# Optimization experiments

Measured on AMD Instinct MI355X. Metric: run time of the kernel, lower is better.

The kernel has to match this reference:

```python
import jax, jax.numpy as jnp
import numpy as np

K = 256       # num states
M = 2         # markov order
D = 256       # lemb_size
V = 50000     # ntypes (vocab)
T = 512
B = 256
Kp1 = K + 1
EPS = 1e-5
INIT = 0.1


def _layernorm(h, g, b):
    mu = h.mean(-1, keepdims=True)
    var = ((h - mu) ** 2).mean(-1, keepdims=True)
    return (h - mu) / jnp.sqrt(var + EPS) * g + b


def setup_inputs() -> dict:
    key = jax.random.key(0)
    ks = jax.random.split(key, 12)
    u = lambda k, shp: jax.random.uniform(k, shp, jnp.float32, -INIT, INIT)
    return {
        "x": jax.random.randint(ks[0], (T, B), 0, V, dtype=jnp.int32),
        "z": jax.random.randint(ks[1], (T, B), 0, K, dtype=jnp.int32),
        "lembs": u(ks[2], (K, D)),
        "tlembs": u(ks[3], (Kp1, D)),
        "dec_W": u(ks[4], (V, D)),
        "dec_b": jnp.zeros((V,), jnp.float32),
        "em_W": u(ks[5], (D, D)),
        "em_bias": jnp.zeros((D,), jnp.float32),
        "em_g": jnp.ones((D,), jnp.float32),
        "em_beta": jnp.zeros((D,), jnp.float32),
        "td_W": u(ks[6], (K, M * D)),
        "td_b": jnp.zeros((K,), jnp.float32),
        "tm_W": u(ks[7], (M * D, M * D)),
        "tm_bias": jnp.zeros((M * D,), jnp.float32),
        "tn_g": jnp.ones((M * D,), jnp.float32),
        "tn_beta": jnp.zeros((M * D,), jnp.float32),
    }


def reference(x, z, lembs, tlembs, dec_W, dec_b, em_W, em_bias, em_g, em_beta,
              td_W, td_b, tm_W, tm_bias, tn_g, tn_beta):
    # --- emission distribution: K x V log-normalized ---
    h = _layernorm(lembs + jax.nn.relu(lembs @ em_W.T + em_bias), em_g, em_beta)
    emdist = jax.nn.log_softmax(h @ dec_W.T + dec_b, axis=1)  # (K, V)

    # --- transition distribution: (Kp1^M, K) log-normalized ---
    # cartesian product of label embeddings, row-major: row r <-> (i_0,...,i_{M-1})
    idx = jnp.indices((Kp1,) * M).reshape(M, -1)                 # (M, Kp1^M)
    cat = tlembs[idx].transpose(1, 0, 2).reshape(-1, M * D)      # (Kp1^M, M*D)
    th = _layernorm(cat + jax.nn.relu(cat @ tm_W.T + tm_bias), tn_g, tn_beta)
    transdist = jax.nn.log_softmax(th @ td_W.T + td_b, axis=1)   # (Kp1^M, K)

    # --- log_joint ---
    xlps = emdist.T[x]                                           # (T, B, K)
    emlps = jnp.take_along_axis(xlps, z[..., None].astype(jnp.int32), axis=2)[..., 0].sum(0)  # (B,)

    zpad = jnp.concatenate([jnp.full((M, B), K, dtype=z.dtype), z], axis=0)  # (T+M, B)
    win = jnp.stack([zpad[m:m + T] for m in range(M + 1)], 0)    # (M+1, T, B)
    lin = win[0]
    for m in range(1, M):
        lin = lin * Kp1 + win[m]                                 # row index into (Kp1^M, K)
    trans_lps = transdist[lin, win[M]]                           # (T, B)
    return emlps + trans_lps.sum(0)                              # (B,)
```

## Files before the change

kernel.cpp:

```cpp
#include <hip/hip_runtime.h>

#define Kst 256
#define Dd 256
#define Vv 50000
#define VPAD 50176
#define Tt 512
#define Bb 256
#define KP1 257
#define MD 512
#define NROWS (KP1*KP1)
#define EPSf 1e-5f

#define VB2 196
#define NP1 (VB2*4)
#define NTR ((NROWS+31)/32)
#define EMB 800

typedef __attribute__((ext_vector_type(8))) short short8;
typedef __attribute__((ext_vector_type(4))) float f32x4;
typedef __attribute__((ext_vector_type(4))) unsigned u32x4;
typedef __attribute__((ext_vector_type(2))) unsigned u32x2;

__device__ __forceinline__ unsigned short f2bf(float f) {
    unsigned u = __builtin_bit_cast(unsigned, f);
    unsigned r = (u + 0x7fffu + ((u >> 16) & 1u)) >> 16;
    return (unsigned short)r;
}
__device__ __forceinline__ float bf2f(unsigned short u) {
    return __builtin_bit_cast(float, ((unsigned)u) << 16);
}
__device__ __forceinline__ unsigned bfpack(float lo, float hi) {
    return __builtin_amdgcn_perm(__builtin_bit_cast(unsigned, hi),
                                 __builtin_bit_cast(unsigned, lo), 0x07060302u);
}
__device__ __forceinline__ unsigned f2bf2(float lo, float hi) {
    return (unsigned)f2bf(lo) | ((unsigned)f2bf(hi) << 16);
}

__global__ __launch_bounds__(256) void k_pack(
    const float* __restrict__ dec_W, unsigned short* __restrict__ dwP,
    const float* __restrict__ em_W, unsigned short* __restrict__ emWP,
    const float* __restrict__ tm_W, unsigned short* __restrict__ tmWP,
    const float* __restrict__ td_W, const float* __restrict__ tn_g,
    const float* __restrict__ tn_beta, const float* __restrict__ td_b,
    unsigned short* __restrict__ tdwg_bf, float* __restrict__ Gt,
    float* __restrict__ Bt)
{
    __shared__ short pl[64][266];
    int bid = blockIdx.x;
    int tid = threadIdx.x, lane = tid & 63, wv = tid >> 6;

    if (bid < 784) {
        int vb2 = bid >> 2, c = bid & 3;
        int base_row = vb2*256 + c*64;
        #pragma unroll 4
        for (int i = 0; i < 16; ++i) {
            int row = wv*16 + i;
            int grow = base_row + row; if (grow > Vv-1) grow = Vv-1;
            float4 f = ((const float4*)(dec_W + (size_t)grow*Dd))[lane];
            u32x2 w; w.x = bfpack(f.x, f.y); w.y = bfpack(f.z, f.w);
            *(u32x2*)&pl[row][lane*4] = w;
        }
        __syncthreads();
        #pragma unroll
        for (int i = 0; i < 8; ++i) {
            short8 val = *(const short8*)&pl[(lane & 15)*4 + wv][i*32 + (lane >> 4)*8];
            *(short8*)(dwP + ((size_t)vb2*8192 + (size_t)i*1024
                              + (c*4 + wv)*64 + lane)*8) = val;
        }
        return;
    }
    if (bid < 788) {
        int jc = bid - 784;
        #pragma unroll 4
        for (int i = 0; i < 16; ++i) {
            int row = wv*16 + i;
            int j = jc*64 + row;
            float4 f = ((const float4*)(em_W + (size_t)j*Dd))[lane];
            u32x2 w; w.x = bfpack(f.x, f.y); w.y = bfpack(f.z, f.w);
            *(u32x2*)&pl[row][lane*4] = w;
        }
        __syncthreads();
        #pragma unroll
        for (int i = 0; i < 8; ++i) {
            short8 val = *(const short8*)&pl[(lane & 15)*4 + wv][i*32 + (lane >> 4)*8];
            *(short8*)(emWP + ((size_t)(i*16 + jc*4 + wv)*64 + lane)*8) = val;
        }
        return;
    }
    if (bid < 804) {
        int idx = bid - 788;
        int jb = idx >> 3, t = idx & 7, jc = t >> 1, kh = t & 1;
        #pragma unroll 4
        for (int i = 0; i < 16; ++i) {
            int row = wv*16 + i;
            int j = jb*256 + jc*64 + row;
            float4 f = ((const float4*)(tm_W + (size_t)j*MD + kh*256))[lane];
            u32x2 w; w.x = bfpack(f.x, f.y); w.y = bfpack(f.z, f.w);
            *(u32x2*)&pl[row][lane*4] = w;
        }
        __syncthreads();
        #pragma unroll
        for (int i = 0; i < 8; ++i) {
            int ksG = kh*8 + i;
            short8 val = *(const short8*)&pl[(lane & 15)*4 + wv][i*32 + (lane >> 4)*8];
            *(short8*)(tmWP + ((size_t)((jb*16 + ksG)*16 + jc*4 + wv)*64 + lane)*8) = val;
        }
        return;
    }
    {
        int c = (bid - 804)*4 + wv;
        const float4* w4 = (const float4*)(td_W + (size_t)c*MD);
        const float4* g4 = (const float4*)tn_g;
        const float4* b4 = (const float4*)tn_beta;
        float sg = 0.f, sb = 0.f;
        short8 o;
        #pragma unroll
        for (int u = 0; u < 2; ++u) {
            int j4 = lane*2 + u;
            float4 w = w4[j4], g = g4[j4], bt = b4[j4];
            sg += w.x*g.x + w.y*g.y + w.z*g.z + w.w*g.w;
            sb += w.x*bt.x + w.y*bt.y + w.z*bt.z + w.w*bt.w;
            o[u*4+0] = (short)f2bf(w.x*g.x);
            o[u*4+1] = (short)f2bf(w.y*g.y);
            o[u*4+2] = (short)f2bf(w.z*g.z);
            o[u*4+3] = (short)f2bf(w.w*g.w);
        }
        {
            int wvv = c >> 6, l15v = (c >> 2) & 15, ctv = c & 3;
            int ksv = lane >> 2, qv = lane & 3;
            *(short8*)(tdwg_bf +
                ((((size_t)wvv*16 + ksv)*4 + ctv)*64 + (qv*16 + l15v))*8) = o;
        }
        #pragma unroll
        for (int dd = 32; dd > 0; dd >>= 1) {
            sg += __shfl_xor(sg, dd);
            sb += __shfl_xor(sb, dd);
        }
        if (lane == 0) { Gt[c] = sg; Bt[c] = sb + td_b[c]; }
    }
}

__global__ __launch_bounds__(256) void k_hP2(
    const float* __restrict__ lembs, const float* __restrict__ em_bias,
    const float* __restrict__ em_g, const float* __restrict__ em_beta,
    unsigned short* __restrict__ h_bf, const float* __restrict__ tlembs,
    float* __restrict__ P0, float* __restrict__ P1,
    const unsigned short* __restrict__ emWP, const unsigned short* __restrict__ tmWP)
{
    __shared__ short ta[32][264];
    __shared__ float lsep[4][32][2];
    __shared__ float musig[32][2];
    int bid = blockIdx.x;
    int tid = threadIdx.x, lane = tid & 63, wv = tid >> 6;
    int l15 = lane & 15, q = lane >> 4;

    int job, r0, cb;
    const float* Arow;
    const short8* bb8;
    if (bid < 8) {
        job = 0; r0 = bid*32; cb = 0;
        Arow = lembs;
        bb8 = (const short8*)emWP + (size_t)(wv*4)*64 + lane;
    } else {
        int b2 = bid - 8;
        int half = b2 / 18;
        int b3 = b2 % 18;
        job = 1 + half;
        r0 = (b3 >> 1) * 32;
        cb = (b3 & 1) * 256;
        int jb = cb >> 8;
        Arow = tlembs;
        bb8 = (const short8*)tmWP + ((size_t)(jb*16 + half*8)*16 + wv*4)*64 + lane;
    }

    {
        int row = tid >> 3, seg = (tid & 7) * 32;
        int r = r0 + row;
        if (r > 256) r = 256;
        const float4* s4 = (const float4*)(Arow + (size_t)r*Dd + seg);
        #pragma unroll
        for (int u = 0; u < 4; ++u) {
            float4 f0 = s4[u*2], f1 = s4[u*2+1];
            u32x4 pk;
            pk.x = bfpack(f0.x, f0.y);
            pk.y = bfpack(f0.z, f0.w);
            pk.z = bfpack(f1.x, f1.y);
            pk.w = bfpack(f1.z, f1.w);
            *(short8*)&ta[row][seg + u*8] = __builtin_bit_cast(short8, pk);
        }
    }
    __syncthreads();

    f32x4 acc[2][4];
    #pragma unroll
    for (int rt = 0; rt < 2; ++rt)
        #pragma unroll
        for (int ct = 0; ct < 4; ++ct)
            acc[rt][ct] = (f32x4){0.f,0.f,0.f,0.f};
    #pragma unroll
    for (int ks = 0; ks < 8; ++ks) {
        short8 a0 = *(const short8*)&ta[ 0 + l15][ks*32 + q*8];
        short8 a1 = *(const short8*)&ta[16 + l15][ks*32 + q*8];
        short8 b0 = bb8[(ks*16 + 0)*64];
        short8 b1 = bb8[(ks*16 + 1)*64];
        short8 b2 = bb8[(ks*16 + 2)*64];
        short8 b3 = bb8[(ks*16 + 3)*64];
        acc[0][0] = __builtin_amdgcn_mfma_f32_16x16x32_bf16(a0, b0, acc[0][0], 0,0,0);
        acc[1][0] = __builtin_amdgcn_mfma_f32_16x16x32_bf16(a1, b0, acc[1][0], 0,0,0);
        acc[0][1] = __builtin_amdgcn_mfma_f32_16x16x32_bf16(a0, b1, acc[0][1], 0,0,0);
        acc[1][1] = __builtin_amdgcn_mfma_f32_16x16x32_bf16(a1, b1, acc[1][1], 0,0,0);
        acc[0][2] = __builtin_amdgcn_mfma_f32_16x16x32_bf16(a0, b2, acc[0][2], 0,0,0);
        acc[1][2] = __builtin_amdgcn_mfma_f32_16x16x32_bf16(a1, b2, acc[1][2], 0,0,0);
        acc[0][3] = __builtin_amdgcn_mfma_f32_16x16x32_bf16(a0, b3, acc[0][3], 0,0,0);
        acc[1][3] = __builtin_amdgcn_mfma_f32_16x16x32_bf16(a1, b3, acc[1][3], 0,0,0);
    }

    if (job != 0) {
        float* Pd = (job == 1) ? P0 : P1;
        #pragma unroll
        for (int rt = 0; rt < 2; ++rt) {
            #pragma unroll
            for (int reg = 0; reg < 4; ++reg) {
                int r = r0 + rt*16 + q*4 + reg;
                if (r < KP1) {
                    float4 o;
                    o.x = acc[rt][0][reg]; o.y = acc[rt][1][reg];
                    o.z = acc[rt][2][reg]; o.w = acc[rt][3][reg];
                    *(float4*)(Pd + (size_t)r*MD + cb + wv*64 + l15*4) = o;
                }
            }
        }
        return;
    }

    float4 bias4 = *(const float4*)(em_bias + wv*64 + l15*4);
    #pragma unroll
    for (int rt = 0; rt < 2; ++rt) {
        #pragma unroll
        for (int reg = 0; reg < 4; ++reg) {
            int r = r0 + rt*16 + q*4 + reg;
            float4 lv = *(const float4*)(lembs + (size_t)r*Dd + wv*64 + l15*4);
            acc[rt][0][reg] = lv.x + fmaxf(acc[rt][0][reg] + bias4.x, 0.f);
            acc[rt][1][reg] = lv.y + fmaxf(acc[rt][1][reg] + bias4.y, 0.f);
            acc[rt][2][reg] = lv.z + fmaxf(acc[rt][2][reg] + bias4.z, 0.f);
            acc[rt][3][reg] = lv.w + fmaxf(acc[rt][3][reg] + bias4.w, 0.f);
        }
    }
    #pragma unroll
    for (int rt = 0; rt < 2; ++rt) {
        #pragma unroll
        for (int reg = 0; reg < 4; ++reg) {
            float s  = ((acc[rt][0][reg] + acc[rt][1][reg]) + (acc[rt][2][reg] + acc[rt][3][reg]));
            float ss = ((acc[rt][0][reg]*acc[rt][0][reg] + acc[rt][1][reg]*acc[rt][1][reg])
                      + (acc[rt][2][reg]*acc[rt][2][reg] + acc[rt][3][reg]*acc[rt][3][reg]));
            s  += __shfl_xor(s, 1);  ss += __shfl_xor(ss, 1);
            s  += __shfl_xor(s, 2);  ss += __shfl_xor(ss, 2);
            s  += __shfl_xor(s, 4);  ss += __shfl_xor(ss, 4);
            s  += __shfl_xor(s, 8);  ss += __shfl_xor(ss, 8);
            if (l15 == 0) {
                int rw = rt*16 + q*4 + reg;
                lsep[wv][rw][0] = s;
                lsep[wv][rw][1] = ss;
            }
        }
    }
    __syncthreads();
    if (tid < 32) {
        float s  = (lsep[0][tid][0] + lsep[1][tid][0]) + (lsep[2][tid][0] + lsep[3][tid][0]);
        float ss = (lsep[0][tid][1] + lsep[1][tid][1]) + (lsep[2][tid][1] + lsep[3][tid][1]);
        float mu = s * (1.f/Dd);
        musig[tid][0] = mu;
        musig[tid][1] = rsqrtf(ss*(1.f/Dd) - mu*mu + EPSf);
    }
    __syncthreads();
    float4 g4  = *(const float4*)(em_g + wv*64 + l15*4);
    float4 be4 = *(const float4*)(em_beta + wv*64 + l15*4);
    #pragma unroll
    for (int rt = 0; rt < 2; ++rt) {
        #pragma unroll
        for (int reg = 0; reg < 4; ++reg) {
            int rw = rt*16 + q*4 + reg;
            int r = r0 + rw;
            float mu = musig[rw][0], rs = musig[rw][1];
            float e0 = (acc[rt][0][reg] - mu)*rs*g4.x + be4.x;
            float e1 = (acc[rt][1][reg] - mu)*rs*g4.y + be4.y;
            float e2 = (acc[rt][2][reg] - mu)*rs*g4.z + be4.z;
            float e3 = (acc[rt][3][reg] - mu)*rs*g4.w + be4.w;
            u32x2 p;
            p.x = f2bf2(e0, e1);
            p.y = f2bf2(e2, e3);
            *(u32x2*)(h_bf + (size_t)r*Dd + wv*64 + l15*4) = p;
        }
    }
}

union SMemU {
    struct { short hs[64][264]; } em;
    struct { short th[32][520]; float musig[32][2]; float lsep[4][32][2]; } tr;
};

__global__ __launch_bounds__(256, 4) void k_emtrans(
    const unsigned short* __restrict__ dwP, const float* __restrict__ dec_b,
    const unsigned short* __restrict__ h_bf, float* __restrict__ part1,
    unsigned short* __restrict__ E2,
    const float* __restrict__ tlembs, const float* __restrict__ P0,
    const float* __restrict__ P1, const float* __restrict__ tm_bias,
    const short* __restrict__ tdwg_bf, const float* __restrict__ Gt,
    const float* __restrict__ Bt, float* __restrict__ lse_t,
    unsigned short* __restrict__ Td)
{
    __shared__ SMemU sm;
    int bid = blockIdx.x;
    int tid = threadIdx.x, lane = tid & 63, wv = tid >> 6;
    int l15 = lane & 15, q = lane >> 4;

    if (bid < EMB) {
        int xcd = bid & 7, slot = bid >> 3;
        int g2 = slot >> 2, kg = slot & 3;
        int vb = g2*8 + xcd;
        if (vb >= VB2) return;
        short (*hs)[264] = sm.em.hs;

        {
            int row = tid >> 2, c0 = (tid & 3) * 64;
            const short8* src = (const short8*)(h_bf + (size_t)(kg*64 + row)*Dd + c0);
            #pragma unroll
            for (int u = 0; u < 8; ++u)
                *(short8*)&hs[row][c0 + u*8] = src[u];
        }
        __syncthreads();

        f32x4 acc[4][4];
        #pragma unroll
        for (int mt = 0; mt < 4; ++mt)
            #pragma unroll
            for (int ct = 0; ct < 4; ++ct)
                acc[mt][ct] = (f32x4){0.f,0.f,0.f,0.f};

        const short8* bb8 = (const short8*)dwP + ((size_t)vb*8*16 + wv*4)*64 + lane;
        short8 Bf[3][4];
        #define LDB_EM(slot_, kk) { \
            Bf[slot_][0] = bb8[((kk)*16 + 0)*64]; \
            Bf[slot_][1] = bb8[((kk)*16 + 1)*64]; \
            Bf[slot_][2] = bb8[((kk)*16 + 2)*64]; \
            Bf[slot_][3] = bb8[((kk)*16 + 3)*64]; }
        LDB_EM(0, 0)
        LDB_EM(1, 1)
        #pragma unroll
        for (int ks = 0; ks < 8; ++ks) {
            if (ks < 6) LDB_EM((ks+2)%3, ks+2)
            short8 a[4];
            #pragma unroll
            for (int mt = 0; mt < 4; ++mt)
                a[mt] = *(const short8*)&hs[mt*16 + l15][ks*32 + q*8];
            #pragma unroll
            for (int mt = 0; mt < 4; ++mt)
                #pragma unroll
                for (int ct = 0; ct < 4; ++ct)
                    acc[mt][ct] = __builtin_amdgcn_mfma_f32_16x16x32_bf16(a[mt], Bf[ks%3][ct], acc[mt][ct], 0,0,0);
        }
        #undef LDB_EM

        int vcol[4]; bool vok[4];
        #pragma unroll
        for (int ct = 0; ct < 4; ++ct) {
            int v = vb*256 + wv*64 + l15*4 + ct;
            vok[ct] = (v < Vv);
            vcol[ct] = v < Vv ? v : Vv-1;
        }
        #pragma unroll
        for (int ct = 0; ct < 4; ++ct) {
            if (vok[ct]) {
                float db = dec_b[vcol[ct]];
                #pragma unroll
                for (int mt = 0; mt < 4; ++mt)
                    #pragma unroll
                    for (int reg = 0; reg < 4; ++reg)
                        acc[mt][ct][reg] += db;
            } else {
                #pragma unroll
                for (int mt = 0; mt < 4; ++mt)
                    #pragma unroll
                    for (int reg = 0; reg < 4; ++reg)
                        acc[mt][ct][reg] = -1e30f;
            }
        }
        #pragma unroll
        for (int mt = 0; mt < 4; ++mt) {
            #pragma unroll
            for (int reg = 0; reg < 4; ++reg) {
                int k = kg*64 + mt*16 + q*4 + reg;
                u32x2 p;
                p.x = f2bf2(acc[mt][0][reg], acc[mt][1][reg]);
                p.y = f2bf2(acc[mt][2][reg], acc[mt][3][reg]);
                *(u32x2*)(E2 + (size_t)k*VPAD + vb*256 + wv*64 + l15*4) = p;
            }
        }
        #pragma unroll
        for (int mt = 0; mt < 4; ++mt) {
            #pragma unroll
            for (int reg = 0; reg < 4; ++reg) {
                float s = (__expf(acc[mt][0][reg]) + __expf(acc[mt][1][reg]))
                        + (__expf(acc[mt][2][reg]) + __expf(acc[mt][3][reg]));
                s += __shfl_xor(s, 1);
                s += __shfl_xor(s, 2);
                s += __shfl_xor(s, 4);
                s += __shfl_xor(s, 8);
                if (l15 == 0) {
                    int k = kg*64 + mt*16 + q*4 + reg;
                    part1[(size_t)(vb*4 + wv)*256 + k] = s;
                }
            }
        }
        return;
    }

    int tr_id = bid - EMB;
    if (tr_id >= NTR) return;
    short (*th)[520]   = sm.tr.th;
    float (*musig)[2]  = sm.tr.musig;
    float (*lsep)[32][2] = sm.tr.lsep;
    int r0 = tr_id * 32;

    {
        const float4* bias0 = (const float4*)tm_bias;
        const float4* bias1 = (const float4*)(tm_bias + 256);
        float4 c0 = bias0[lane], c1 = bias1[lane];
        int i0a[8], i1a[8];
        #pragma unroll
        for (int i = 0; i < 8; ++i) {
            int r = r0 + wv*8 + i; if (r >= NROWS) r = NROWS - 1;
            i0a[i] = r / KP1; i1a[i] = r - i0a[i]*KP1;
        }
        #define ROWBODY(i, A0, B0, T0, A1, B1, T1) { \
            int row = wv*8 + (i); \
            float v0 = (T0).x + fmaxf((A0).x+(B0).x+c0.x, 0.f); \
            float v1 = (T0).y + fmaxf((A0).y+(B0).y+c0.y, 0.f); \
            float v2 = (T0).z + fmaxf((A0).z+(B0).z+c0.z, 0.f); \
            float v3 = (T0).w + fmaxf((A0).w+(B0).w+c0.w, 0.f); \
            float v4 = (T1).x + fmaxf((A1).x+(B1).x+c1.x, 0.f); \
            float v5 = (T1).y + fmaxf((A1).y+(B1).y+c1.y, 0.f); \
            float v6 = (T1).z + fmaxf((A1).z+(B1).z+c1.z, 0.f); \
            float v7 = (T1).w + fmaxf((A1).w+(B1).w+c1.w, 0.f); \
            u32x2 p0; p0.x = bfpack(v0, v1); p0.y = bfpack(v2, v3); \
            u32x2 p1; p1.x = bfpack(v4, v5); p1.y = bfpack(v6, v7); \
            *(u32x2*)&th[row][lane*4]       = p0; \
            *(u32x2*)&th[row][256 + lane*4] = p1; \
            float s  = ((v0+v1)+(v2+v3)) + ((v4+v5)+(v6+v7)); \
            float ss = ((v0*v0+v1*v1)+(v2*v2+v3*v3)) + ((v4*v4+v5*v5)+(v6*v6+v7*v7)); \
            _Pragma("unroll") \
            for (int d = 1; d < 64; d <<= 1) { \
                s  += __shfl_xor(s, d); \
                ss += __shfl_xor(ss, d); \
            } \
            if (lane == 0) { \
                float mu = s * (1.f/MD); \
                musig[row][0] = mu; \
                musig[row][1] = rsqrtf(ss*(1.f/MD) - mu*mu + EPSf); \
            } }

        if (i0a[0] == i0a[7]) {
            float4 A0 = ((const float4*)(P0 + (size_t)i0a[0]*MD))[lane];
            float4 A1 = ((const float4*)(P0 + (size_t)i0a[0]*MD + 256))[lane];
            float4 T0 = ((const float4*)(tlembs + (size_t)i0a[0]*Dd))[lane];
            #pragma unroll
            for (int i = 0; i < 8; ++i) {
                float4 b0 = ((const float4*)(P1 + (size_t)i1a[i]*MD))[lane];
                float4 b1 = ((const float4*)(P1 + (size_t)i1a[i]*MD + 256))[lane];
                float4 t1 = ((const float4*)(tlembs + (size_t)i1a[i]*Dd))[lane];
                ROWBODY(i, A0, b0, T0, A1, b1, t1)
            }
        } else {
            #pragma unroll
            for (int i = 0; i < 8; ++i) {
                float4 A0 = ((const float4*)(P0 + (size_t)i0a[i]*MD))[lane];
                float4 A1 = ((const float4*)(P0 + (size_t)i0a[i]*MD + 256))[lane];
                float4 T0 = ((const float4*)(tlembs + (size_t)i0a[i]*Dd))[lane];
                float4 b0 = ((const float4*)(P1 + (size_t)i1a[i]*MD))[lane];
                float4 b1 = ((const float4*)(P1 + (size_t)i1a[i]*MD + 256))[lane];
                float4 t1 = ((const float4*)(tlembs + (size_t)i1a[i]*Dd))[lane];
                ROWBODY(i, A0, b0, T0, A1, b1, t1)
            }
        }
        #undef ROWBODY
    }
    __syncthreads();

    f32x4 acc[2][4];
    #pragma unroll
    for (int rt = 0; rt < 2; ++rt)
        #pragma unroll
        for (int ct = 0; ct < 4; ++ct)
            acc[rt][ct] = (f32x4){0.f, 0.f, 0.f, 0.f};
    const short* bb = tdwg_bf + (size_t)wv*32768 + (size_t)lane*8;
    short8 Bf[3][4];
    #define LDB_TR(slot_, kk) { const short* nxt = bb + (size_t)(kk)*2048; \
        Bf[slot_][0] = *(const short8*)(nxt); \
        Bf[slot_][1] = *(const short8*)(nxt + 512); \
        Bf[slot_][2] = *(const short8*)(nxt + 1024); \
        Bf[slot_][3] = *(const short8*)(nxt + 1536); }
    LDB_TR(0, 0)
    LDB_TR(1, 1)
    #pragma unroll
    for (int ks = 0; ks < 16; ++ks) {
        if (ks < 14) LDB_TR((ks+2)%3, ks+2)
        int ko = ks*32 + q*8;
        short8 a0 = *(const short8*)&th[ 0 + l15][ko];
        short8 a1 = *(const short8*)&th[16 + l15][ko];
        acc[0][0] = __builtin_amdgcn_mfma_f32_16x16x32_bf16(a0, Bf[ks%3][0], acc[0][0], 0,0,0);
        acc[1][0] = __builtin_amdgcn_mfma_f32_16x16x32_bf16(a1, Bf[ks%3][0], acc[1][0], 0,0,0);
        acc[0][1] = __builtin_amdgcn_mfma_f32_16x16x32_bf16(a0, Bf[ks%3][1], acc[0][1], 0,0,0);
        acc[1][1] = __builtin_amdgcn_mfma_f32_16x16x32_bf16(a1, Bf[ks%3][1], acc[1][1], 0,0,0);
        acc[0][2] = __builtin_amdgcn_mfma_f32_16x16x32_bf16(a0, Bf[ks%3][2], acc[0][2], 0,0,0);
        acc[1][2] = __builtin_amdgcn_mfma_f32_16x16x32_bf16(a1, Bf[ks%3][2], acc[1][2], 0,0,0);
        acc[0][3] = __builtin_amdgcn_mfma_f32_16x16x32_bf16(a0, Bf[ks%3][3], acc[0][3], 0,0,0);
        acc[1][3] = __builtin_amdgcn_mfma_f32_16x16x32_bf16(a1, Bf[ks%3][3], acc[1][3], 0,0,0);
    }
    #undef LDB_TR

    float4 Gc = *(const float4*)(Gt + wv*64 + l15*4);
    float4 Bc = *(const float4*)(Bt + wv*64 + l15*4);
    #pragma unroll
    for (int rt = 0; rt < 2; ++rt) {
        #pragma unroll
        for (int reg = 0; reg < 4; ++reg) {
            int rw = rt*16 + q*4 + reg;
            float mu = musig[rw][0], rs = musig[rw][1];
            float e0 = rs*(acc[rt][0][reg] - mu*Gc.x) + Bc.x;
            float e1 = rs*(acc[rt][1][reg] - mu*Gc.y) + Bc.y;
            float e2 = rs*(acc[rt][2][reg] - mu*Gc.z) + Bc.z;
            float e3 = rs*(acc[rt][3][reg] - mu*Gc.w) + Bc.w;
            long r = (long)r0 + rw;
            if (r < NROWS) {
                u32x2 p;
                p.x = f2bf2(e0, e1);
                p.y = f2bf2(e2, e3);
                *(u32x2*)(Td + (size_t)r*Kst + wv*64 + l15*4) = p;
            }
            float m = fmaxf(fmaxf(e0, e1), fmaxf(e2, e3));
            m = fmaxf(m, __shfl_xor(m, 1));
            m = fmaxf(m, __shfl_xor(m, 2));
            m = fmaxf(m, __shfl_xor(m, 4));
            m = fmaxf(m, __shfl_xor(m, 8));
            float s = __expf(e0 - m) + __expf(e1 - m) + __expf(e2 - m) + __expf(e3 - m);
            s += __shfl_xor(s, 1);
            s += __shfl_xor(s, 2);
            s += __shfl_xor(s, 4);
            s += __shfl_xor(s, 8);
            if (l15 == 0) {
                lsep[wv][rw][0] = m;
                lsep[wv][rw][1] = s;
            }
        }
    }
    __syncthreads();
    if (tid < 32) {
        int r = r0 + tid;
        if (r < NROWS) {
            float m0 = lsep[0][tid][0], m1 = lsep[1][tid][0];
            float m2 = lsep[2][tid][0], m3 = lsep[3][tid][0];
            float mg = fmaxf(fmaxf(m0, m1), fmaxf(m2, m3));
            float s = lsep[0][tid][1]*__expf(m0-mg) + lsep[1][tid][1]*__expf(m1-mg)
                    + lsep[2][tid][1]*__expf(m2-mg) + lsep[3][tid][1]*__expf(m3-mg);
            lse_t[r] = mg + logf(s);
        }
    }
}

__global__ __launch_bounds__(256) void k_lse8(
    const float* __restrict__ part1, float* __restrict__ lpart)
{
    __shared__ float lemp[4][256];
    int tid = threadIdx.x, lane = tid & 63, w = tid >> 6;
    const f32x4* p4 = (const f32x4*)part1;
    f32x4 s4 = (f32x4){0.f,0.f,0.f,0.f};
    int j0 = blockIdx.x * 98;
    for (int j = j0 + w; j < j0 + 98; j += 4) {
        f32x4 v = p4[(size_t)j*64 + lane];
        s4.x += v.x; s4.y += v.y; s4.z += v.z; s4.w += v.w;
    }
    *(f32x4*)&lemp[w][lane*4] = s4;
    __syncthreads();
    lpart[blockIdx.x*256 + tid] = (lemp[0][tid] + lemp[1][tid]) + (lemp[2][tid] + lemp[3][tid]);
}

__global__ __launch_bounds__(256) void k_gather7(
    const int* __restrict__ x, const int* __restrict__ z,
    const unsigned short* __restrict__ E2, const float* __restrict__ lpart,
    const unsigned short* __restrict__ Td, const float* __restrict__ lse_t,
    float* __restrict__ gpart)
{
    __shared__ float lem[256];
    int tid = threadIdx.x;
    {
        float s = 0.f;
        #pragma unroll
        for (int r = 0; r < 8; ++r) s += lpart[r*256 + tid];
        lem[tid] = logf(s);
    }
    __syncthreads();

    int b = tid;
    int t0 = blockIdx.x * 8;
    int zm1 = (t0 >= 1) ? z[(t0-1)*Bb + b] : Kst;
    int zm2 = (t0 >= 2) ? z[(t0-2)*Bb + b] : Kst;
    float accv = 0.f;
    #pragma unroll
    for (int u = 0; u < 8; ++u) {
        int t = t0 + u;
        int zc = z[t*Bb + b];
        int xv = x[t*Bb + b];
        int lin = zm2*KP1 + zm1;
        accv += bf2f(E2[(size_t)zc*VPAD + xv]) - lem[zc]
              + bf2f(Td[(size_t)lin*Kst + zc]) - lse_t[lin];
        zm2 = zm1; zm1 = zc;
    }
    gpart[blockIdx.x*Bb + b] = accv;
}

__global__ __launch_bounds__(256) void k_fin(
    const float* __restrict__ gpart, float* __restrict__ out)
{
    int b = threadIdx.x;
    float s = 0.f;
    #pragma unroll 8
    for (int r = 0; r < 64; ++r)
        s += gpart[r*Bb + b];
    out[b] = s;
}

extern "C" void kernel_launch(void* const* d_in, const int* in_sizes, int n_in,
                              void* d_out, int out_size, void* d_ws, size_t ws_size,
                              hipStream_t stream)
{
    const int*   x       = (const int*)  d_in[0];
    const int*   z       = (const int*)  d_in[1];
    const float* lembs   = (const float*)d_in[2];
    const float* tlembs  = (const float*)d_in[3];
    const float* dec_W   = (const float*)d_in[4];
    const float* dec_b   = (const float*)d_in[5];
    const float* em_W    = (const float*)d_in[6];
    const float* em_bias = (const float*)d_in[7];
    const float* em_g    = (const float*)d_in[8];
    const float* em_beta = (const float*)d_in[9];
    const float* td_W    = (const float*)d_in[10];
    const float* td_b    = (const float*)d_in[11];
    const float* tm_W    = (const float*)d_in[12];
    const float* tm_bias = (const float*)d_in[13];
    const float* tn_g    = (const float*)d_in[14];
    const float* tn_beta = (const float*)d_in[15];
    float* out = (float*)d_out;

    float* ws     = (float*)d_ws;
    float* P0     = ws;
    float* P1     = P0 + 131584;
    float* part1  = P1 + 131584;
    float* lpart  = part1 + 200704;
    float* gpart  = lpart + 2048;
    float* lse_t  = gpart + 16384;
    float* Gt     = lse_t + 66052;
    float* Bt     = Gt + 256;
    unsigned short* tdwg_bf = (unsigned short*)(Bt + 256);
    unsigned short* h_bf   = tdwg_bf + 131072;
    unsigned short* E2     = h_bf + 65536;
    unsigned short* Td     = E2 + (size_t)Kst*VPAD;
    unsigned short* dwP    = Td + (size_t)NROWS*Kst;
    unsigned short* emWP   = dwP + (size_t)VPAD*Kst;
    unsigned short* tmWP   = emWP + 65536;

    k_pack<<<868, 256, 0, stream>>>(dec_W, dwP, em_W, emWP, tm_W, tmWP,
                                    td_W, tn_g, tn_beta, td_b, tdwg_bf, Gt, Bt);
    k_hP2<<<44, 256, 0, stream>>>(lembs, em_bias, em_g, em_beta, h_bf,
                                  tlembs, P0, P1, emWP, tmWP);
    k_emtrans<<<EMB + NTR, 256, 0, stream>>>(
        dwP, dec_b, h_bf, part1, E2,
        tlembs, P0, P1, tm_bias, (const short*)tdwg_bf, Gt, Bt, lse_t, Td);
    k_lse8<<<8, 256, 0, stream>>>(part1, lpart);
    k_gather7<<<64, 256, 0, stream>>>(x, z, E2, lpart, Td, lse_t, gpart);
    k_fin<<<1, 256, 0, stream>>>(gpart, out);
}
```

Baseline: 210.9 us.

## Fuse emission/transition lookups into producing tiles via pre-bucketed queries

Adds a bucketing kernel that uses atomics to group every (t,b) query by the emission tile (z block, vocab block) and the transition row block it needs. The emission and transition tiles now stage their bf16 log-prob results in shared memory and answer the bucketed queries there, writing per-token values. This removes the global E2 (K×V) and Td (Kp1²×K) tables and the scattered gather over them. In exchange it adds a memset, a small atomic-heavy kernel and extra syncs, and fixed bucket capacities silently drop queries if input skew overflows them.

```diff
diff --git a/kernel.cpp b/kernel.cpp
--- a/kernel.cpp
+++ b/kernel.cpp
@@ -15,6 +15,8 @@
 #define NP1 (VB2*4)
 #define NTR ((NROWS+31)/32)
 #define EMB 800
+#define EBCAP 512
+#define TBCAP 512
 
 typedef __attribute__((ext_vector_type(8))) short short8;
 typedef __attribute__((ext_vector_type(4))) float f32x4;
@@ -35,6 +37,30 @@
 }
 __device__ __forceinline__ unsigned f2bf2(float lo, float hi) {
     return (unsigned)f2bf(lo) | ((unsigned)f2bf(hi) << 16);
+}
+
+__global__ __launch_bounds__(256) void k_bucket(
+    const int* __restrict__ x, const int* __restrict__ z,
+    int* __restrict__ cntE, int* __restrict__ bktE,
+    int* __restrict__ cntT, int* __restrict__ bktT)
+{
+    int b = threadIdx.x;
+    int t0 = blockIdx.x * 4;
+    #pragma unroll
+    for (int u = 0; u < 4; ++u) {
+        int t = t0 + u;
+        int zc = z[t*Bb + b];
+        int xv = x[t*Bb + b];
+        int i0 = (t >= 2) ? z[(t-2)*Bb + b] : Kst;
+        int i1 = (t >= 1) ? z[(t-1)*Bb + b] : Kst;
+        int lin = i0*KP1 + i1;
+        int eb = (zc >> 6)*VB2 + (xv >> 8);
+        int ie = atomicAdd(&cntE[eb], 1);
+        if (ie < EBCAP) bktE[(size_t)eb*EBCAP + ie] = t*Bb + b;
+        int tb2 = lin >> 5;
+        int it = atomicAdd(&cntT[tb2], 1);
+        if (it < TBCAP) bktT[(size_t)tb2*TBCAP + it] = t*Bb + b;
+    }
 }
 
 __global__ __launch_bounds__(256) void k_pack(
@@ -303,12 +329,14 @@
 __global__ __launch_bounds__(256, 4) void k_emtrans(
     const unsigned short* __restrict__ dwP, const float* __restrict__ dec_b,
     const unsigned short* __restrict__ h_bf, float* __restrict__ part1,
-    unsigned short* __restrict__ E2,
     const float* __restrict__ tlembs, const float* __restrict__ P0,
     const float* __restrict__ P1, const float* __restrict__ tm_bias,
     const short* __restrict__ tdwg_bf, const float* __restrict__ Gt,
-    const float* __restrict__ Bt, float* __restrict__ lse_t,
-    unsigned short* __restrict__ Td)
+    const float* __restrict__ Bt,
+    const int* __restrict__ x, const int* __restrict__ z,
+    const int* __restrict__ cntE, const int* __restrict__ bktE,
+    const int* __restrict__ cntT, const int* __restrict__ bktT,
+    float* __restrict__ emv, float* __restrict__ trv)
 {
     __shared__ SMemU sm;
     int bid = blockIdx.x;
@@ -362,17 +390,11 @@
         }
         #undef LDB_EM
 
-        int vcol[4]; bool vok[4];
         #pragma unroll
         for (int ct = 0; ct < 4; ++ct) {
             int v = vb*256 + wv*64 + l15*4 + ct;
-            vok[ct] = (v < Vv);
-            vcol[ct] = v < Vv ? v : Vv-1;
-        }
-        #pragma unroll
-        for (int ct = 0; ct < 4; ++ct) {
-            if (vok[ct]) {
-                float db = dec_b[vcol[ct]];
+            if (v < Vv) {
+                float db = dec_b[v];
                 #pragma unroll
                 for (int mt = 0; mt < 4; ++mt)
                     #pragma unroll
@@ -386,15 +408,16 @@
                         acc[mt][ct][reg] = -1e30f;
             }
         }
+        __syncthreads();
         #pragma unroll
         for (int mt = 0; mt < 4; ++mt) {
             #pragma unroll
             for (int reg = 0; reg < 4; ++reg) {
-                int k = kg*64 + mt*16 + q*4 + reg;
+                int kl = mt*16 + q*4 + reg;
                 u32x2 p;
                 p.x = f2bf2(acc[mt][0][reg], acc[mt][1][reg]);
                 p.y = f2bf2(acc[mt][2][reg], acc[mt][3][reg]);
-                *(u32x2*)(E2 + (size_t)k*VPAD + vb*256 + wv*64 + l15*4) = p;
+                *(u32x2*)&hs[kl][wv*64 + l15*4] = p;
             }
         }
         #pragma unroll
@@ -411,6 +434,18 @@
                     int k = kg*64 + mt*16 + q*4 + reg;
                     part1[(size_t)(vb*4 + wv)*256 + k] = s;
                 }
+            }
+        }
+        __syncthreads();
+        {
+            int bk = kg*VB2 + vb;
+            int nb = cntE[bk]; if (nb > EBCAP) nb = EBCAP;
+            const int* lst = bktE + (size_t)bk*EBCAP;
+            for (int i = tid; i < nb; i += 256) {
+                int tb = lst[i];
+                int zc = z[tb];
+                int xv = x[tb];
+                emv[tb] = bf2f((unsigned short)hs[zc & 63][xv & 255]);
             }
         }
         return;
@@ -521,6 +556,7 @@
 
     float4 Gc = *(const float4*)(Gt + wv*64 + l15*4);
     float4 Bc = *(const float4*)(Bt + wv*64 + l15*4);
+    __syncthreads();
     #pragma unroll
     for (int rt = 0; rt < 2; ++rt) {
         #pragma unroll
@@ -531,13 +567,10 @@
             float e1 = rs*(acc[rt][1][reg] - mu*Gc.y) + Bc.y;
             float e2 = rs*(acc[rt][2][reg] - mu*Gc.z) + Bc.z;
             float e3 = rs*(acc[rt][3][reg] - mu*Gc.w) + Bc.w;
-            long r = (long)r0 + rw;
-            if (r < NROWS) {
-                u32x2 p;
-                p.x = f2bf2(e0, e1);
-                p.y = f2bf2(e2, e3);
-                *(u32x2*)(Td + (size_t)r*Kst + wv*64 + l15*4) = p;
-            }
+            u32x2 p;
+            p.x = f2bf2(e0, e1);
+            p.y = f2bf2(e2, e3);
+            *(u32x2*)&th[rw][wv*64 + l15*4] = p;
             float m = fmaxf(fmaxf(e0, e1), fmaxf(e2, e3));
             m = fmaxf(m, __shfl_xor(m, 1));
             m = fmaxf(m, __shfl_xor(m, 2));
@@ -556,14 +589,25 @@
     }
     __syncthreads();
     if (tid < 32) {
-        int r = r0 + tid;
-        if (r < NROWS) {
-            float m0 = lsep[0][tid][0], m1 = lsep[1][tid][0];
-            float m2 = lsep[2][tid][0], m3 = lsep[3][tid][0];
-            float mg = fmaxf(fmaxf(m0, m1), fmaxf(m2, m3));
-            float s = lsep[0][tid][1]*__expf(m0-mg) + lsep[1][tid][1]*__expf(m1-mg)
-                    + lsep[2][tid][1]*__expf(m2-mg) + lsep[3][tid][1]*__expf(m3-mg);
-            lse_t[r] = mg + logf(s);
+        float m0 = lsep[0][tid][0], m1 = lsep[1][tid][0];
+        float m2 = lsep[2][tid][0], m3 = lsep[3][tid][0];
+        float mg = fmaxf(fmaxf(m0, m1), fmaxf(m2, m3));
+        float s = lsep[0][tid][1]*__expf(m0-mg) + lsep[1][tid][1]*__expf(m1-mg)
+                + lsep[2][tid][1]*__expf(m2-mg) + lsep[3][tid][1]*__expf(m3-mg);
+        musig[tid][0] = mg + logf(s);
+    }
+    __syncthreads();
+    {
+        int nb = cntT[tr_id]; if (nb > TBCAP) nb = TBCAP;
+        const int* lst = bktT + (size_t)tr_id*TBCAP;
+        for (int i = tid; i < nb; i += 256) {
+            int tb = lst[i];
+            int t = tb >> 8;
+            int zc = z[tb];
+            int i0 = (t >= 2) ? z[tb - 2*Bb] : Kst;
+            int i1 = (t >= 1) ? z[tb - Bb] : Kst;
+            int rl = i0*KP1 + i1 - r0;
+            trv[tb] = bf2f((unsigned short)th[rl][zc]) - musig[rl][0];
         }
     }
 }
@@ -585,10 +629,9 @@
     lpart[blockIdx.x*256 + tid] = (lemp[0][tid] + lemp[1][tid]) + (lemp[2][tid] + lemp[3][tid]);
 }
 
-__global__ __launch_bounds__(256) void k_gather7(
-    const int* __restrict__ x, const int* __restrict__ z,
-    const unsigned short* __restrict__ E2, const float* __restrict__ lpart,
-    const unsigned short* __restrict__ Td, const float* __restrict__ lse_t,
+__global__ __launch_bounds__(256) void k_gather8(
+    const int* __restrict__ z, const float* __restrict__ emv,
+    const float* __restrict__ trv, const float* __restrict__ lpart,
     float* __restrict__ gpart)
 {
     __shared__ float lem[256];
@@ -603,18 +646,12 @@
 
     int b = tid;
     int t0 = blockIdx.x * 8;
-    int zm1 = (t0 >= 1) ? z[(t0-1)*Bb + b] : Kst;
-    int zm2 = (t0 >= 2) ? z[(t0-2)*Bb + b] : Kst;
     float accv = 0.f;
     #pragma unroll
     for (int u = 0; u < 8; ++u) {
-        int t = t0 + u;
-        int zc = z[t*Bb + b];
-        int xv = x[t*Bb + b];
-        int lin = zm2*KP1 + zm1;
-        accv += bf2f(E2[(size_t)zc*VPAD + xv]) - lem[zc]
-              + bf2f(Td[(size_t)lin*Kst + zc]) - lse_t[lin];
-        zm2 = zm1; zm1 = zc;
+        int tb = (t0 + u)*Bb + b;
+        int zc = z[tb];
+        accv += emv[tb] - lem[zc] + trv[tb];
     }
     gpart[blockIdx.x*Bb + b] = accv;
 }
@@ -658,25 +695,31 @@
     float* part1  = P1 + 131584;
     float* lpart  = part1 + 200704;
     float* gpart  = lpart + 2048;
-    float* lse_t  = gpart + 16384;
-    float* Gt     = lse_t + 66052;
+    float* Gt     = gpart + 16384;
     float* Bt     = Gt + 256;
-    unsigned short* tdwg_bf = (unsigned short*)(Bt + 256);
+    float* emv    = Bt + 256;
+    float* trv    = emv + 131072;
+    int*   cntE   = (int*)(trv + 131072);
+    int*   cntT   = cntE + 784;
+    int*   bktE   = cntT + 2065;
+    int*   bktT   = bktE + (size_t)784*EBCAP;
+    unsigned short* tdwg_bf = (unsigned short*)(bktT + (size_t)NTR*TBCAP);
     unsigned short* h_bf   = tdwg_bf + 131072;
-    unsigned short* E2     = h_bf + 65536;
-    unsigned short* Td     = E2 + (size_t)Kst*VPAD;
-    unsigned short* dwP    = Td + (size_t)NROWS*Kst;
-    unsigned short* emWP   = dwP + (size_t)VPAD*Kst;
+    unsigned short* emWP   = h_bf + 65536;
     unsigned short* tmWP   = emWP + 65536;
-
+    unsigned short* dwP    = tmWP + 262144;
+
+    hipMemsetAsync(cntE, 0, (784 + 2065)*sizeof(int), stream);
+    k_bucket<<<Tt/4, 256, 0, stream>>>(x, z, cntE, bktE, cntT, bktT);
     k_pack<<<868, 256, 0, stream>>>(dec_W, dwP, em_W, emWP, tm_W, tmWP,
                                     td_W, tn_g, tn_beta, td_b, tdwg_bf, Gt, Bt);
     k_hP2<<<44, 256, 0, stream>>>(lembs, em_bias, em_g, em_beta, h_bf,
                                   tlembs, P0, P1, emWP, tmWP);
     k_emtrans<<<EMB + NTR, 256, 0, stream>>>(
-        dwP, dec_b, h_bf, part1, E2,
-        tlembs, P0, P1, tm_bias, (const short*)tdwg_bf, Gt, Bt, lse_t, Td);
+        dwP, dec_b, h_bf, part1,
+        tlembs, P0, P1, tm_bias, (const short*)tdwg_bf, Gt, Bt,
+        x, z, cntE, bktE, cntT, bktT, emv, trv);
     k_lse8<<<8, 256, 0, stream>>>(part1, lpart);
-    k_gather7<<<64, 256, 0, stream>>>(x, z, E2, lpart, Td, lse_t, gpart);
+    k_gather8<<<64, 256, 0, stream>>>(z, emv, trv, lpart, gpart);
     k_fin<<<1, 256, 0, stream>>>(gpart, out);
 }
```

Result: slower. 244.3 us (+15.8%).
